# Optimization experiments

Hardware: AMD Instinct MI355X
Metric: run time of the kernel (lower is better)

## Reference

```python
import jax, jax.numpy as jnp
import numpy as np

# OmniNet(deepqmc) reconstruction: ElectronicSchNet v1 (2 interactions, kernel_dim=8,
# embedding_dim=16, dist_feat_dim=4) + Linear(16,1,bias=False) orbital + sum over electrons.
# SchNet v1: shared w and g per interaction, spin-dependent h (same/anti), nuclear
# messages via learned nuclear embeddings Y. Subnets: w = 2-layer log-DNN 4->6->8 with SSP,
# h = Linear(16,8), g = Linear(8,16). SSP(x) = softplus(x) - log(2).

N_UP, N_DOWN = 16, 16
N_ELEC = N_UP + N_DOWN
N_ATOMS = 8
DIST_FEAT, KERNEL, EMBED = 4, 8, 16
N_INTER = 2
BATCH = 4096


def ssp(x):
    return jax.nn.softplus(x) - jnp.log(2.0).astype(x.dtype)


def setup_inputs() -> dict:
    key = jax.random.key(0)
    ks = jax.random.split(key, 16)
    s = 0.5  # init scale
    return {
        'dists_nuc': jax.random.uniform(ks[0], (BATCH, N_ELEC, N_ATOMS, DIST_FEAT), jnp.float32),
        'dists_elec': jax.random.uniform(ks[1], (BATCH, N_ELEC, N_ELEC, DIST_FEAT), jnp.float32),
        'X': jax.random.normal(ks[2], (1, EMBED), jnp.float32) * s,          # electron embedding (n_up==n_down)
        'Y': jax.random.normal(ks[3], (N_ATOMS, KERNEL), jnp.float32) * s,   # nuclear embeddings
        'w1': jax.random.normal(ks[4], (N_INTER, DIST_FEAT, 6), jnp.float32) * s,
        'wb1': jax.random.normal(ks[5], (N_INTER, 6), jnp.float32) * s,
        'w2': jax.random.normal(ks[6], (N_INTER, 6, KERNEL), jnp.float32) * s,
        'wb2': jax.random.normal(ks[7], (N_INTER, KERNEL), jnp.float32) * s,
        'hs_w': jax.random.normal(ks[8], (N_INTER, EMBED, KERNEL), jnp.float32) * s,
        'hs_b': jax.random.normal(ks[9], (N_INTER, KERNEL), jnp.float32) * s,
        'ha_w': jax.random.normal(ks[10], (N_INTER, EMBED, KERNEL), jnp.float32) * s,
        'ha_b': jax.random.normal(ks[11], (N_INTER, KERNEL), jnp.float32) * s,
        'g_w': jax.random.normal(ks[12], (N_INTER, KERNEL, EMBED), jnp.float32) * s,
        'g_b': jax.random.normal(ks[13], (N_INTER, EMBED), jnp.float32) * s,
        'orb_w': jax.random.normal(ks[14], (EMBED,), jnp.float32) * s,
    }


def reference(dists_nuc, dists_elec, X, Y, w1, wb1, w2, wb2, hs_w, hs_b, ha_w, ha_b, g_w, g_b, orb_w):
    B, n_elec = dists_elec.shape[:2]
    dt = dists_elec.dtype
    spins = jnp.concatenate([jnp.zeros(N_UP, jnp.int32), jnp.ones(N_DOWN, jnp.int32)])
    eye = jnp.eye(n_elec, dtype=bool)
    same = ((spins[:, None] == spins[None, :]) & ~eye).astype(dt)  # (i,j) same-spin, no self
    anti = (spins[:, None] != spins[None, :]).astype(dt)

    # initial embeddings: all electrons share X[0] since n_up == n_down
    x = jnp.broadcast_to(X[0], (B, n_elec, EMBED))

    for n in range(N_INTER):
        def w_net(e):  # (..., 4) -> (..., 8)
            return ssp(e @ w1[n] + wb1[n]) @ w2[n] + wb2[n]
        we = w_net(dists_elec)            # (B, i, j, K)
        wn = w_net(dists_nuc)             # (B, i, M, K)
        hs = x @ hs_w[n] + hs_b[n]        # (B, j, K) same-spin message features
        ha = x @ ha_w[n] + ha_b[n]        # (B, j, K) anti-spin
        z = (jnp.einsum('bijk,ij,bjk->bik', we, same, hs)
             + jnp.einsum('bijk,ij,bjk->bik', we, anti, ha)
             + jnp.einsum('bimk,mk->bik', wn, Y))
        x = x + (z @ g_w[n] + g_b[n])     # residual update

    # orbital projection (Linear(16,1,bias=False)), squeeze, sum over electrons
    return (x @ orb_w).sum(axis=-1)       # (B,)
```

## Files before the change

kernel.cpp:

```cpp
#include <hip/hip_runtime.h>

#define NE 32
#define NA 8
#define DF 4
#define KD 8
#define ED 16
#define BATCH 4096

#define WS_W1S0 0
#define WS_W1S1 24
#define WS_B1S0 48
#define WS_B1S1 54
#define WS_B2H0 60
#define WS_B2H1 68
#define WS_MS0  76
#define WS_MA0  84
#define WS_MS   92
#define WS_MA   156
#define WS_CS   220
#define WS_CA   228
#define WS_GO0  236
#define WS_GO1  244
#define WS_BASE 252

__global__ void omni_setup(const float* __restrict__ X,   const float* __restrict__ w1,
                           const float* __restrict__ wb1, const float* __restrict__ w2,
                           const float* __restrict__ wb2, const float* __restrict__ hs_w,
                           const float* __restrict__ hs_b,const float* __restrict__ ha_w,
                           const float* __restrict__ ha_b,const float* __restrict__ g_w,
                           const float* __restrict__ g_b, const float* __restrict__ orb_w,
                           float* __restrict__ ws)
{
    const int t = threadIdx.x;
    const float L   = 1.4426950408889634f;
    const float LN2 = 0.6931471805599453f;
    if (t < 48) {
        ws[t] = w1[t] * L;
    } else if (t < 60) {
        ws[t] = wb1[t - 48] * L;
    } else if (t < 76) {
        const int u = t - 60, n = u >> 3, k = u & 7;
        float sw = 0.f;
        for (int a = 0; a < 6; ++a) sw += w2[n * 48 + a * KD + k];
        ws[t] = wb2[n * KD + k] * L - sw;
    } else if (t < 92) {
        const int u = t - 76, tab = u >> 3, k = u & 7;
        const float* mw = tab ? ha_w : hs_w;
        const float* mb = tab ? ha_b : hs_b;
        float acc = mb[k];
        for (int c = 0; c < ED; ++c) acc += X[c] * mw[c * KD + k];
        ws[t] = acc;
    } else if (t < 220) {
        int u = t - 92; const int tab = u >> 6; u &= 63;
        const int kp = u >> 3, k = u & 7;
        const float* mw = (tab ? ha_w : hs_w) + ED * KD;
        float acc = 0.f;
        for (int c = 0; c < ED; ++c)
            acc += LN2 * g_w[kp * ED + c] * mw[c * KD + k];
        ws[t] = acc;
    } else if (t < 236) {
        const int u = t - 220, tab = u >> 3, k = u & 7;
        const float* mw = (tab ? ha_w : hs_w) + ED * KD;
        const float* mb = (tab ? ha_b : hs_b) + KD;
        float acc = mb[k];
        for (int c = 0; c < ED; ++c) acc += (X[c] + g_b[c]) * mw[c * KD + k];
        ws[t] = acc;
    } else if (t < 252) {
        const int u = t - 236, n = u >> 3, k = u & 7;
        float acc = 0.f;
        for (int c = 0; c < ED; ++c)
            acc += LN2 * g_w[n * KD * ED + k * ED + c] * orb_w[c];
        ws[t] = acc;
    } else if (t == 252) {
        float acc = 0.f;
        for (int c = 0; c < ED; ++c) acc += (X[c] + g_b[c] + g_b[ED + c]) * orb_w[c];
        ws[t] = acc;
    }
}

__device__ __forceinline__ void wnet(const float4 e,
                                     const float* __restrict__ vB1s,
                                     const float* __restrict__ vB2h,
                                     const float* __restrict__ sW1,
                                     const float* __restrict__ sW2,
                                     float* __restrict__ racc)
{
    float r[6];
    #pragma unroll
    for (int a = 0; a < 6; ++a) {
        float u = fmaf(e.x, sW1[a], vB1s[a]);
        u = fmaf(e.y, sW1[6 + a], u);
        u = fmaf(e.z, sW1[12 + a], u);
        u = fmaf(e.w, sW1[18 + a], u);
        r[a] = __builtin_amdgcn_logf(__builtin_amdgcn_exp2f(u) + 1.0f);
    }
    #pragma unroll
    for (int k = 0; k < KD; ++k) {
        float acc = fmaf(r[0], sW2[k], vB2h[k]);
        #pragma unroll
        for (int a = 1; a < 6; ++a) acc = fmaf(r[a], sW2[a * KD + k], acc);
        racc[k] = acc;
    }
}

__global__ __launch_bounds__(128, 4) void omni_main(
    const float* __restrict__ dists_nuc,
    const float* __restrict__ dists_elec,
    const float* __restrict__ Y,
    const float* __restrict__ w2,
    const float* __restrict__ ws,
    float* __restrict__ out)
{
    const int tid  = threadIdx.x;
    const int h    = tid >> 6;
    const int lane = tid & 63;
    const int il   = lane & 15;
    const int jh   = lane >> 4;
    const int ig   = 16 * h + il;
    const int b    = blockIdx.x;
    const int sj   = jh >> 1;
    const bool same = (sj == h);
    const int t32  = same ? 0 : 32;

    __shared__ float msg[65][KD];
    __shared__ float part[2];
    if (tid < KD) msg[64][tid] = 0.0f;

    const float* de = dists_elec + (((size_t)b * NE + ig) * NE + 8 * jh) * DF;
    const float* dn = dists_nuc  + (((size_t)b * NE + ig) * NA + 2 * jh) * DF;
    float4 E[8];
    #pragma unroll
    for (int s = 0; s < 8; ++s) E[s] = ((const float4*)de)[s];
    const float4 F0 = ((const float4*)dn)[0];
    const float4 F1 = ((const float4*)dn)[1];
    const float4 Ya0 = ((const float4*)Y)[4 * jh + 0];
    const float4 Ya1 = ((const float4*)Y)[4 * jh + 1];
    const float4 Yb0 = ((const float4*)Y)[4 * jh + 2];
    const float4 Yb1 = ((const float4*)Y)[4 * jh + 3];

    float zr0[KD];
    {
        float vB1s[6], vB2h[KD], msel[KD];
        #pragma unroll
        for (int a = 0; a < 6; ++a) vB1s[a] = ws[WS_B1S0 + a];
        #pragma unroll
        for (int k = 0; k < KD; ++k) vB2h[k] = ws[WS_B2H0 + k];
        #pragma unroll
        for (int k = 0; k < KD; ++k) msel[k] = same ? ws[WS_MS0 + k] : ws[WS_MA0 + k];

        float zacc[KD];
        #pragma unroll
        for (int k = 0; k < KD; ++k) zacc[k] = 0.0f;
        const int scnt = ig - 8 * jh;
        #pragma unroll
        for (int s = 0; s < 8; ++s) {
            float racc[KD];
            wnet(E[s], vB1s, vB2h, ws + WS_W1S0, w2, racc);
            const float mf = (s == scnt) ? 0.0f : 1.0f;
            #pragma unroll
            for (int k = 0; k < KD; ++k) zacc[k] = fmaf(racc[k], mf, zacc[k]);
        }
        float z[KD];
        #pragma unroll
        for (int k = 0; k < KD; ++k) z[k] = zacc[k] * msel[k];
        {
            float racc[KD];
            wnet(F0, vB1s, vB2h, ws + WS_W1S0, w2, racc);
            z[0] = fmaf(racc[0], Ya0.x, z[0]); z[1] = fmaf(racc[1], Ya0.y, z[1]);
            z[2] = fmaf(racc[2], Ya0.z, z[2]); z[3] = fmaf(racc[3], Ya0.w, z[3]);
            z[4] = fmaf(racc[4], Ya1.x, z[4]); z[5] = fmaf(racc[5], Ya1.y, z[5]);
            z[6] = fmaf(racc[6], Ya1.z, z[6]); z[7] = fmaf(racc[7], Ya1.w, z[7]);
            wnet(F1, vB1s, vB2h, ws + WS_W1S0, w2, racc);
            z[0] = fmaf(racc[0], Yb0.x, z[0]); z[1] = fmaf(racc[1], Yb0.y, z[1]);
            z[2] = fmaf(racc[2], Yb0.z, z[2]); z[3] = fmaf(racc[3], Yb0.w, z[3]);
            z[4] = fmaf(racc[4], Yb1.x, z[4]); z[5] = fmaf(racc[5], Yb1.y, z[5]);
            z[6] = fmaf(racc[6], Yb1.z, z[6]); z[7] = fmaf(racc[7], Yb1.w, z[7]);
        }
        #pragma unroll
        for (int k = 0; k < KD; ++k) {
            z[k] += __shfl_xor(z[k], 16, 64);
            z[k] += __shfl_xor(z[k], 32, 64);
            zr0[k] = z[k];
        }
    }

    {
        float ms[KD], ma[KD];
        #pragma unroll
        for (int k = 0; k < KD; ++k) {
            float as = zr0[0] * ws[WS_MS + k];
            float aa = zr0[0] * ws[WS_MA + k];
            #pragma unroll
            for (int kp = 1; kp < KD; ++kp) {
                as = fmaf(zr0[kp], ws[WS_MS + kp * KD + k], as);
                aa = fmaf(zr0[kp], ws[WS_MA + kp * KD + k], aa);
            }
            ms[k] = as + ws[WS_CS + k];
            ma[k] = aa + ws[WS_CA + k];
        }
        if (jh == 0) {
            #pragma unroll
            for (int k = 0; k < KD; ++k) msg[ig][k] = ms[k];
        } else if (jh == 2) {
            #pragma unroll
            for (int k = 0; k < KD; ++k) msg[32 + ig][k] = ma[k];
        }
        __syncthreads();
    }

    float zr1[KD];
    {
        float vB1s[6], vB2h[KD];
        #pragma unroll
        for (int a = 0; a < 6; ++a) vB1s[a] = ws[WS_B1S1 + a];
        #pragma unroll
        for (int k = 0; k < KD; ++k) vB2h[k] = ws[WS_B2H1 + k];

        float z[KD];
        #pragma unroll
        for (int k = 0; k < KD; ++k) z[k] = 0.0f;
        #pragma unroll
        for (int s = 0; s < 8; ++s) {
            float racc[KD];
            wnet(E[s], vB1s, vB2h, ws + WS_W1S1, w2 + 48, racc);
            const int j = 8 * jh + s;
            const int row = (j == ig) ? 64 : (t32 + j);
            const float4 m0 = *(const float4*)&msg[row][0];
            const float4 m1 = *(const float4*)&msg[row][4];
            z[0] = fmaf(racc[0], m0.x, z[0]); z[1] = fmaf(racc[1], m0.y, z[1]);
            z[2] = fmaf(racc[2], m0.z, z[2]); z[3] = fmaf(racc[3], m0.w, z[3]);
            z[4] = fmaf(racc[4], m1.x, z[4]); z[5] = fmaf(racc[5], m1.y, z[5]);
            z[6] = fmaf(racc[6], m1.z, z[6]); z[7] = fmaf(racc[7], m1.w, z[7]);
        }
        {
            float racc[KD];
            wnet(F0, vB1s, vB2h, ws + WS_W1S1, w2 + 48, racc);
            z[0] = fmaf(racc[0], Ya0.x, z[0]); z[1] = fmaf(racc[1], Ya0.y, z[1]);
            z[2] = fmaf(racc[2], Ya0.z, z[2]); z[3] = fmaf(racc[3], Ya0.w, z[3]);
            z[4] = fmaf(racc[4], Ya1.x, z[4]); z[5] = fmaf(racc[5], Ya1.y, z[5]);
            z[6] = fmaf(racc[6], Ya1.z, z[6]); z[7] = fmaf(racc[7], Ya1.w, z[7]);
            wnet(F1, vB1s, vB2h, ws + WS_W1S1, w2 + 48, racc);
            z[0] = fmaf(racc[0], Yb0.x, z[0]); z[1] = fmaf(racc[1], Yb0.y, z[1]);
            z[2] = fmaf(racc[2], Yb0.z, z[2]); z[3] = fmaf(racc[3], Yb0.w, z[3]);
            z[4] = fmaf(racc[4], Yb1.x, z[4]); z[5] = fmaf(racc[5], Yb1.y, z[5]);
            z[6] = fmaf(racc[6], Yb1.z, z[6]); z[7] = fmaf(racc[7], Yb1.w, z[7]);
        }
        #pragma unroll
        for (int k = 0; k < KD; ++k) {
            z[k] += __shfl_xor(z[k], 16, 64);
            z[k] += __shfl_xor(z[k], 32, 64);
            zr1[k] = z[k];
        }
    }

    float dot = 0.0f;
    #pragma unroll
    for (int k = 0; k < KD; ++k) dot = fmaf(zr0[k], ws[WS_GO0 + k], dot);
    #pragma unroll
    for (int k = 0; k < KD; ++k) dot = fmaf(zr1[k], ws[WS_GO1 + k], dot);
    dot += ws[WS_BASE];
    dot *= 0.25f;
    #pragma unroll
    for (int off = 1; off < 64; off <<= 1) dot += __shfl_xor(dot, off, 64);
    if (lane == 0) part[h] = dot;
    __syncthreads();
    if (tid == 0) out[b] = part[0] + part[1];
}

extern "C" void kernel_launch(void* const* d_in, const int* in_sizes, int n_in,
                              void* d_out, int out_size, void* d_ws, size_t ws_size,
                              hipStream_t stream) {
    const float* dists_nuc  = (const float*)d_in[0];
    const float* dists_elec = (const float*)d_in[1];
    const float* X     = (const float*)d_in[2];
    const float* Y     = (const float*)d_in[3];
    const float* w1    = (const float*)d_in[4];
    const float* wb1   = (const float*)d_in[5];
    const float* w2    = (const float*)d_in[6];
    const float* wb2   = (const float*)d_in[7];
    const float* hs_w  = (const float*)d_in[8];
    const float* hs_b  = (const float*)d_in[9];
    const float* ha_w  = (const float*)d_in[10];
    const float* ha_b  = (const float*)d_in[11];
    const float* g_w   = (const float*)d_in[12];
    const float* g_b   = (const float*)d_in[13];
    const float* orb_w = (const float*)d_in[14];
    float* out = (float*)d_out;
    float* ws  = (float*)d_ws;

    omni_setup<<<1, 256, 0, stream>>>(X, w1, wb1, w2, wb2, hs_w, hs_b,
                                      ha_w, ha_b, g_w, g_b, orb_w, ws);
    omni_main<<<BATCH, 128, 0, stream>>>(dists_nuc, dists_elec, Y, w2, ws, out);
}
```

Baseline: 156.3 us.

## Sum first-interaction SSP features before projection and pack two samples per block

In the first interaction the per-pair message is linear in the SSP hidden layer, so the kernel now sums the six hidden activations over j and applies the 6->8 projection once, scaling the bias by the neighbour count. This removes most of the per-pair projection FMAs. Each 256-thread block now handles two batch samples with separate shared buffers, and launch bounds change to 256 threads with 6 waves. The Y loads are moved into the scopes where they are used to shorten register live ranges. The bias scaling relies on the count being 7 or 8, and the occupancy change may shift register pressure.

```diff
diff --git a/kernel.cpp b/kernel.cpp
--- a/kernel.cpp
+++ b/kernel.cpp
@@ -78,14 +78,11 @@
     }
 }
 
-__device__ __forceinline__ void wnet(const float4 e,
-                                     const float* __restrict__ vB1s,
-                                     const float* __restrict__ vB2h,
-                                     const float* __restrict__ sW1,
-                                     const float* __restrict__ sW2,
-                                     float* __restrict__ racc)
+__device__ __forceinline__ void wnet_r(const float4 e,
+                                       const float* __restrict__ vB1s,
+                                       const float* __restrict__ sW1,
+                                       float* __restrict__ r)
 {
-    float r[6];
     #pragma unroll
     for (int a = 0; a < 6; ++a) {
         float u = fmaf(e.x, sW1[a], vB1s[a]);
@@ -94,6 +91,13 @@
         u = fmaf(e.w, sW1[18 + a], u);
         r[a] = __builtin_amdgcn_logf(__builtin_amdgcn_exp2f(u) + 1.0f);
     }
+}
+
+__device__ __forceinline__ void proj(const float* __restrict__ r,
+                                     const float* __restrict__ sW2,
+                                     const float* __restrict__ vB2h,
+                                     float* __restrict__ racc)
+{
     #pragma unroll
     for (int k = 0; k < KD; ++k) {
         float acc = fmaf(r[0], sW2[k], vB2h[k]);
@@ -103,7 +107,7 @@
     }
 }
 
-__global__ __launch_bounds__(128, 4) void omni_main(
+__global__ __launch_bounds__(256, 6) void omni_main(
     const float* __restrict__ dists_nuc,
     const float* __restrict__ dists_elec,
     const float* __restrict__ Y,
@@ -112,19 +116,20 @@
     float* __restrict__ out)
 {
     const int tid  = threadIdx.x;
-    const int h    = tid >> 6;
+    const int el   = tid >> 7;
+    const int h    = (tid >> 6) & 1;
     const int lane = tid & 63;
     const int il   = lane & 15;
     const int jh   = lane >> 4;
     const int ig   = 16 * h + il;
-    const int b    = blockIdx.x;
+    const int b    = blockIdx.x * 2 + el;
     const int sj   = jh >> 1;
     const bool same = (sj == h);
     const int t32  = same ? 0 : 32;
 
-    __shared__ float msg[65][KD];
-    __shared__ float part[2];
-    if (tid < KD) msg[64][tid] = 0.0f;
+    __shared__ float msg[2][65][KD];
+    __shared__ float part[2][2];
+    if (tid < 16) msg[tid >> 3][64][tid & 7] = 0.0f;
 
     const float* de = dists_elec + (((size_t)b * NE + ig) * NE + 8 * jh) * DF;
     const float* dn = dists_nuc  + (((size_t)b * NE + ig) * NA + 2 * jh) * DF;
@@ -133,10 +138,6 @@
     for (int s = 0; s < 8; ++s) E[s] = ((const float4*)de)[s];
     const float4 F0 = ((const float4*)dn)[0];
     const float4 F1 = ((const float4*)dn)[1];
-    const float4 Ya0 = ((const float4*)Y)[4 * jh + 0];
-    const float4 Ya1 = ((const float4*)Y)[4 * jh + 1];
-    const float4 Yb0 = ((const float4*)Y)[4 * jh + 2];
-    const float4 Yb1 = ((const float4*)Y)[4 * jh + 3];
 
     float zr0[KD];
     {
@@ -148,29 +149,39 @@
         #pragma unroll
         for (int k = 0; k < KD; ++k) msel[k] = same ? ws[WS_MS0 + k] : ws[WS_MA0 + k];
 
-        float zacc[KD];
-        #pragma unroll
-        for (int k = 0; k < KD; ++k) zacc[k] = 0.0f;
         const int scnt = ig - 8 * jh;
+        const float fcnt = (jh == (ig >> 3)) ? 7.0f : 8.0f;
+        float S[6] = {0.f, 0.f, 0.f, 0.f, 0.f, 0.f};
         #pragma unroll
         for (int s = 0; s < 8; ++s) {
-            float racc[KD];
-            wnet(E[s], vB1s, vB2h, ws + WS_W1S0, w2, racc);
+            float r[6];
+            wnet_r(E[s], vB1s, ws + WS_W1S0, r);
             const float mf = (s == scnt) ? 0.0f : 1.0f;
             #pragma unroll
-            for (int k = 0; k < KD; ++k) zacc[k] = fmaf(racc[k], mf, zacc[k]);
+            for (int a = 0; a < 6; ++a) S[a] = fmaf(r[a], mf, S[a]);
         }
         float z[KD];
         #pragma unroll
-        for (int k = 0; k < KD; ++k) z[k] = zacc[k] * msel[k];
+        for (int k = 0; k < KD; ++k) {
+            float acc = fmaf(S[0], w2[k], fcnt * vB2h[k]);
+            #pragma unroll
+            for (int a = 1; a < 6; ++a) acc = fmaf(S[a], w2[a * KD + k], acc);
+            z[k] = acc * msel[k];
+        }
         {
-            float racc[KD];
-            wnet(F0, vB1s, vB2h, ws + WS_W1S0, w2, racc);
+            const float4 Ya0 = ((const float4*)Y)[4 * jh + 0];
+            const float4 Ya1 = ((const float4*)Y)[4 * jh + 1];
+            const float4 Yb0 = ((const float4*)Y)[4 * jh + 2];
+            const float4 Yb1 = ((const float4*)Y)[4 * jh + 3];
+            float r[6], racc[KD];
+            wnet_r(F0, vB1s, ws + WS_W1S0, r);
+            proj(r, w2, vB2h, racc);
             z[0] = fmaf(racc[0], Ya0.x, z[0]); z[1] = fmaf(racc[1], Ya0.y, z[1]);
             z[2] = fmaf(racc[2], Ya0.z, z[2]); z[3] = fmaf(racc[3], Ya0.w, z[3]);
             z[4] = fmaf(racc[4], Ya1.x, z[4]); z[5] = fmaf(racc[5], Ya1.y, z[5]);
             z[6] = fmaf(racc[6], Ya1.z, z[6]); z[7] = fmaf(racc[7], Ya1.w, z[7]);
-            wnet(F1, vB1s, vB2h, ws + WS_W1S0, w2, racc);
+            wnet_r(F1, vB1s, ws + WS_W1S0, r);
+            proj(r, w2, vB2h, racc);
             z[0] = fmaf(racc[0], Yb0.x, z[0]); z[1] = fmaf(racc[1], Yb0.y, z[1]);
             z[2] = fmaf(racc[2], Yb0.z, z[2]); z[3] = fmaf(racc[3], Yb0.w, z[3]);
             z[4] = fmaf(racc[4], Yb1.x, z[4]); z[5] = fmaf(racc[5], Yb1.y, z[5]);
@@ -200,10 +211,10 @@
         }
         if (jh == 0) {
             #pragma unroll
-            for (int k = 0; k < KD; ++k) msg[ig][k] = ms[k];
+            for (int k = 0; k < KD; ++k) msg[el][ig][k] = ms[k];
         } else if (jh == 2) {
             #pragma unroll
-            for (int k = 0; k < KD; ++k) msg[32 + ig][k] = ma[k];
+            for (int k = 0; k < KD; ++k) msg[el][32 + ig][k] = ma[k];
         }
         __syncthreads();
     }
@@ -221,25 +232,32 @@
         for (int k = 0; k < KD; ++k) z[k] = 0.0f;
         #pragma unroll
         for (int s = 0; s < 8; ++s) {
-            float racc[KD];
-            wnet(E[s], vB1s, vB2h, ws + WS_W1S1, w2 + 48, racc);
+            float r[6], racc[KD];
+            wnet_r(E[s], vB1s, ws + WS_W1S1, r);
+            proj(r, w2 + 48, vB2h, racc);
             const int j = 8 * jh + s;
             const int row = (j == ig) ? 64 : (t32 + j);
-            const float4 m0 = *(const float4*)&msg[row][0];
-            const float4 m1 = *(const float4*)&msg[row][4];
+            const float4 m0 = *(const float4*)&msg[el][row][0];
+            const float4 m1 = *(const float4*)&msg[el][row][4];
             z[0] = fmaf(racc[0], m0.x, z[0]); z[1] = fmaf(racc[1], m0.y, z[1]);
             z[2] = fmaf(racc[2], m0.z, z[2]); z[3] = fmaf(racc[3], m0.w, z[3]);
             z[4] = fmaf(racc[4], m1.x, z[4]); z[5] = fmaf(racc[5], m1.y, z[5]);
             z[6] = fmaf(racc[6], m1.z, z[6]); z[7] = fmaf(racc[7], m1.w, z[7]);
         }
         {
-            float racc[KD];
-            wnet(F0, vB1s, vB2h, ws + WS_W1S1, w2 + 48, racc);
+            const float4 Ya0 = ((const float4*)Y)[4 * jh + 0];
+            const float4 Ya1 = ((const float4*)Y)[4 * jh + 1];
+            const float4 Yb0 = ((const float4*)Y)[4 * jh + 2];
+            const float4 Yb1 = ((const float4*)Y)[4 * jh + 3];
+            float r[6], racc[KD];
+            wnet_r(F0, vB1s, ws + WS_W1S1, r);
+            proj(r, w2 + 48, vB2h, racc);
             z[0] = fmaf(racc[0], Ya0.x, z[0]); z[1] = fmaf(racc[1], Ya0.y, z[1]);
             z[2] = fmaf(racc[2], Ya0.z, z[2]); z[3] = fmaf(racc[3], Ya0.w, z[3]);
             z[4] = fmaf(racc[4], Ya1.x, z[4]); z[5] = fmaf(racc[5], Ya1.y, z[5]);
             z[6] = fmaf(racc[6], Ya1.z, z[6]); z[7] = fmaf(racc[7], Ya1.w, z[7]);
-            wnet(F1, vB1s, vB2h, ws + WS_W1S1, w2 + 48, racc);
+            wnet_r(F1, vB1s, ws + WS_W1S1, r);
+            proj(r, w2 + 48, vB2h, racc);
             z[0] = fmaf(racc[0], Yb0.x, z[0]); z[1] = fmaf(racc[1], Yb0.y, z[1]);
             z[2] = fmaf(racc[2], Yb0.z, z[2]); z[3] = fmaf(racc[3], Yb0.w, z[3]);
             z[4] = fmaf(racc[4], Yb1.x, z[4]); z[5] = fmaf(racc[5], Yb1.y, z[5]);
@@ -262,9 +280,9 @@
     dot *= 0.25f;
     #pragma unroll
     for (int off = 1; off < 64; off <<= 1) dot += __shfl_xor(dot, off, 64);
-    if (lane == 0) part[h] = dot;
+    if (lane == 0) part[el][h] = dot;
     __syncthreads();
-    if (tid == 0) out[b] = part[0] + part[1];
+    if ((tid & 127) == 0) out[b] = part[el][0] + part[el][1];
 }
 
 extern "C" void kernel_launch(void* const* d_in, const int* in_sizes, int n_in,
@@ -290,5 +308,5 @@
 
     omni_setup<<<1, 256, 0, stream>>>(X, w1, wb1, w2, wb2, hs_w, hs_b,
                                       ha_w, ha_b, g_w, g_b, orb_w, ws);
-    omni_main<<<BATCH, 128, 0, stream>>>(dists_nuc, dists_elec, Y, w2, ws, out);
-}
+    omni_main<<<BATCH / 2, 256, 0, stream>>>(dists_nuc, dists_elec, Y, w2, ws, out);
+}
```

Measured after the change: 163.6 us. +4.6%, slower.

## Pack FMAs into float2 ops and hoist interaction-0 projection out of loop

Applied to the files above, without the earlier changes.

Rewrites the w-net and the message projections with 2-wide float vectors so the compiler can emit packed FP32 FMA instructions, which halves the FMA instruction count. In interaction 0 the second linear layer is applied once to the masked sum of hidden activations, scaled by the neighbor count for the bias, instead of once per electron pair. This removes most of that layer's per-pair work. The risks are packed-math codegen overhead from operand splats and register pressure, plus small changes in floating-point summation order.

```diff
diff --git a/kernel.cpp b/kernel.cpp
--- a/kernel.cpp
+++ b/kernel.cpp
@@ -22,6 +22,12 @@
 #define WS_GO0  236
 #define WS_GO1  244
 #define WS_BASE 252
+
+typedef float f32x2 __attribute__((ext_vector_type(2)));
+__device__ __forceinline__ f32x2 splat2(float s) { f32x2 r; r.x = s; r.y = s; return r; }
+__device__ __forceinline__ f32x2 fma2(f32x2 a, f32x2 b, f32x2 c) {
+    return __builtin_elementwise_fma(a, b, c);
+}
 
 __global__ void omni_setup(const float* __restrict__ X,   const float* __restrict__ w1,
                            const float* __restrict__ wb1, const float* __restrict__ w2,
@@ -78,28 +84,41 @@
     }
 }
 
-__device__ __forceinline__ void wnet(const float4 e,
-                                     const float* __restrict__ vB1s,
-                                     const float* __restrict__ vB2h,
-                                     const float* __restrict__ sW1,
-                                     const float* __restrict__ sW2,
-                                     float* __restrict__ racc)
+__device__ __forceinline__ void wnet_r2(const float4 e,
+                                        const f32x2* __restrict__ vB1s2,
+                                        const f32x2* __restrict__ sW12,
+                                        f32x2* __restrict__ r2)
 {
-    float r[6];
-    #pragma unroll
-    for (int a = 0; a < 6; ++a) {
-        float u = fmaf(e.x, sW1[a], vB1s[a]);
-        u = fmaf(e.y, sW1[6 + a], u);
-        u = fmaf(e.z, sW1[12 + a], u);
-        u = fmaf(e.w, sW1[18 + a], u);
-        r[a] = __builtin_amdgcn_logf(__builtin_amdgcn_exp2f(u) + 1.0f);
-    }
-    #pragma unroll
-    for (int k = 0; k < KD; ++k) {
-        float acc = fmaf(r[0], sW2[k], vB2h[k]);
-        #pragma unroll
-        for (int a = 1; a < 6; ++a) acc = fmaf(r[a], sW2[a * KD + k], acc);
-        racc[k] = acc;
+    #pragma unroll
+    for (int a2 = 0; a2 < 3; ++a2) {
+        f32x2 u = fma2(splat2(e.x), sW12[a2], vB1s2[a2]);
+        u = fma2(splat2(e.y), sW12[3 + a2], u);
+        u = fma2(splat2(e.z), sW12[6 + a2], u);
+        u = fma2(splat2(e.w), sW12[9 + a2], u);
+        f32x2 t;
+        t.x = __builtin_amdgcn_exp2f(u.x);
+        t.y = __builtin_amdgcn_exp2f(u.y);
+        t = t + splat2(1.0f);
+        r2[a2].x = __builtin_amdgcn_logf(t.x);
+        r2[a2].y = __builtin_amdgcn_logf(t.y);
+    }
+}
+
+__device__ __forceinline__ void proj2(const f32x2* __restrict__ r2,
+                                      const f32x2* __restrict__ sW22,
+                                      const f32x2* __restrict__ vB2h2,
+                                      f32x2* __restrict__ racc2)
+{
+    #pragma unroll
+    for (int k2 = 0; k2 < 4; ++k2) {
+        f32x2 acc = vB2h2[k2];
+        acc = fma2(splat2(r2[0].x), sW22[0 * 4 + k2], acc);
+        acc = fma2(splat2(r2[0].y), sW22[1 * 4 + k2], acc);
+        acc = fma2(splat2(r2[1].x), sW22[2 * 4 + k2], acc);
+        acc = fma2(splat2(r2[1].y), sW22[3 * 4 + k2], acc);
+        acc = fma2(splat2(r2[2].x), sW22[4 * 4 + k2], acc);
+        acc = fma2(splat2(r2[2].y), sW22[5 * 4 + k2], acc);
+        racc2[k2] = acc;
     }
 }
 
@@ -126,6 +145,10 @@
     __shared__ float part[2];
     if (tid < KD) msg[64][tid] = 0.0f;
 
+    const f32x2* ws2  = (const f32x2*)ws;
+    const f32x2* w2p0 = (const f32x2*)w2;
+    const f32x2* w2p1 = (const f32x2*)(w2 + 48);
+
     const float* de = dists_elec + (((size_t)b * NE + ig) * NE + 8 * jh) * DF;
     const float* dn = dists_nuc  + (((size_t)b * NE + ig) * NA + 2 * jh) * DF;
     float4 E[8];
@@ -133,123 +156,130 @@
     for (int s = 0; s < 8; ++s) E[s] = ((const float4*)de)[s];
     const float4 F0 = ((const float4*)dn)[0];
     const float4 F1 = ((const float4*)dn)[1];
-    const float4 Ya0 = ((const float4*)Y)[4 * jh + 0];
-    const float4 Ya1 = ((const float4*)Y)[4 * jh + 1];
-    const float4 Yb0 = ((const float4*)Y)[4 * jh + 2];
-    const float4 Yb1 = ((const float4*)Y)[4 * jh + 3];
+    f32x2 Y0[4], Y1[4];
+    #pragma unroll
+    for (int k2 = 0; k2 < 4; ++k2) {
+        Y0[k2] = ((const f32x2*)Y)[(2 * jh) * 4 + k2];
+        Y1[k2] = ((const f32x2*)Y)[(2 * jh + 1) * 4 + k2];
+    }
 
     float zr0[KD];
     {
-        float vB1s[6], vB2h[KD], msel[KD];
-        #pragma unroll
-        for (int a = 0; a < 6; ++a) vB1s[a] = ws[WS_B1S0 + a];
-        #pragma unroll
-        for (int k = 0; k < KD; ++k) vB2h[k] = ws[WS_B2H0 + k];
-        #pragma unroll
-        for (int k = 0; k < KD; ++k) msel[k] = same ? ws[WS_MS0 + k] : ws[WS_MA0 + k];
-
-        float zacc[KD];
-        #pragma unroll
-        for (int k = 0; k < KD; ++k) zacc[k] = 0.0f;
-        const int scnt = ig - 8 * jh;
+        f32x2 vB1s2[3], vB2h2[4], msel2[4];
+        #pragma unroll
+        for (int a2 = 0; a2 < 3; ++a2) vB1s2[a2] = ws2[WS_B1S0 / 2 + a2];
+        #pragma unroll
+        for (int k2 = 0; k2 < 4; ++k2) vB2h2[k2] = ws2[WS_B2H0 / 2 + k2];
+        #pragma unroll
+        for (int k2 = 0; k2 < 4; ++k2)
+            msel2[k2] = same ? ws2[WS_MS0 / 2 + k2] : ws2[WS_MA0 / 2 + k2];
+
+        const int scnt  = ig - 8 * jh;
+        const float fcnt = (jh == (ig >> 3)) ? 7.0f : 8.0f;
+        f32x2 S2[3] = {splat2(0.f), splat2(0.f), splat2(0.f)};
         #pragma unroll
         for (int s = 0; s < 8; ++s) {
-            float racc[KD];
-            wnet(E[s], vB1s, vB2h, ws + WS_W1S0, w2, racc);
+            f32x2 r2[3];
+            wnet_r2(E[s], vB1s2, ws2 + WS_W1S0 / 2, r2);
             const float mf = (s == scnt) ? 0.0f : 1.0f;
             #pragma unroll
-            for (int k = 0; k < KD; ++k) zacc[k] = fmaf(racc[k], mf, zacc[k]);
-        }
-        float z[KD];
-        #pragma unroll
-        for (int k = 0; k < KD; ++k) z[k] = zacc[k] * msel[k];
+            for (int a2 = 0; a2 < 3; ++a2) S2[a2] = fma2(r2[a2], splat2(mf), S2[a2]);
+        }
+        f32x2 z2[4];
+        #pragma unroll
+        for (int k2 = 0; k2 < 4; ++k2) {
+            f32x2 acc = splat2(fcnt) * vB2h2[k2];
+            acc = fma2(splat2(S2[0].x), w2p0[0 * 4 + k2], acc);
+            acc = fma2(splat2(S2[0].y), w2p0[1 * 4 + k2], acc);
+            acc = fma2(splat2(S2[1].x), w2p0[2 * 4 + k2], acc);
+            acc = fma2(splat2(S2[1].y), w2p0[3 * 4 + k2], acc);
+            acc = fma2(splat2(S2[2].x), w2p0[4 * 4 + k2], acc);
+            acc = fma2(splat2(S2[2].y), w2p0[5 * 4 + k2], acc);
+            z2[k2] = acc * msel2[k2];
+        }
         {
-            float racc[KD];
-            wnet(F0, vB1s, vB2h, ws + WS_W1S0, w2, racc);
-            z[0] = fmaf(racc[0], Ya0.x, z[0]); z[1] = fmaf(racc[1], Ya0.y, z[1]);
-            z[2] = fmaf(racc[2], Ya0.z, z[2]); z[3] = fmaf(racc[3], Ya0.w, z[3]);
-            z[4] = fmaf(racc[4], Ya1.x, z[4]); z[5] = fmaf(racc[5], Ya1.y, z[5]);
-            z[6] = fmaf(racc[6], Ya1.z, z[6]); z[7] = fmaf(racc[7], Ya1.w, z[7]);
-            wnet(F1, vB1s, vB2h, ws + WS_W1S0, w2, racc);
-            z[0] = fmaf(racc[0], Yb0.x, z[0]); z[1] = fmaf(racc[1], Yb0.y, z[1]);
-            z[2] = fmaf(racc[2], Yb0.z, z[2]); z[3] = fmaf(racc[3], Yb0.w, z[3]);
-            z[4] = fmaf(racc[4], Yb1.x, z[4]); z[5] = fmaf(racc[5], Yb1.y, z[5]);
-            z[6] = fmaf(racc[6], Yb1.z, z[6]); z[7] = fmaf(racc[7], Yb1.w, z[7]);
-        }
-        #pragma unroll
-        for (int k = 0; k < KD; ++k) {
-            z[k] += __shfl_xor(z[k], 16, 64);
-            z[k] += __shfl_xor(z[k], 32, 64);
-            zr0[k] = z[k];
+            f32x2 r2[3], racc2[4];
+            wnet_r2(F0, vB1s2, ws2 + WS_W1S0 / 2, r2);
+            proj2(r2, w2p0, vB2h2, racc2);
+            #pragma unroll
+            for (int k2 = 0; k2 < 4; ++k2) z2[k2] = fma2(racc2[k2], Y0[k2], z2[k2]);
+            wnet_r2(F1, vB1s2, ws2 + WS_W1S0 / 2, r2);
+            proj2(r2, w2p0, vB2h2, racc2);
+            #pragma unroll
+            for (int k2 = 0; k2 < 4; ++k2) z2[k2] = fma2(racc2[k2], Y1[k2], z2[k2]);
+        }
+        #pragma unroll
+        for (int k2 = 0; k2 < 4; ++k2) {
+            float za = z2[k2].x, zb = z2[k2].y;
+            za += __shfl_xor(za, 16, 64); za += __shfl_xor(za, 32, 64);
+            zb += __shfl_xor(zb, 16, 64); zb += __shfl_xor(zb, 32, 64);
+            zr0[2 * k2] = za; zr0[2 * k2 + 1] = zb;
         }
     }
 
     {
-        float ms[KD], ma[KD];
-        #pragma unroll
-        for (int k = 0; k < KD; ++k) {
-            float as = zr0[0] * ws[WS_MS + k];
-            float aa = zr0[0] * ws[WS_MA + k];
-            #pragma unroll
-            for (int kp = 1; kp < KD; ++kp) {
-                as = fmaf(zr0[kp], ws[WS_MS + kp * KD + k], as);
-                aa = fmaf(zr0[kp], ws[WS_MA + kp * KD + k], aa);
+        f32x2 ms2[4], ma2[4];
+        #pragma unroll
+        for (int k2 = 0; k2 < 4; ++k2) {
+            ms2[k2] = ws2[WS_CS / 2 + k2];
+            ma2[k2] = ws2[WS_CA / 2 + k2];
+        }
+        #pragma unroll
+        for (int kp = 0; kp < KD; ++kp) {
+            const f32x2 zk = splat2(zr0[kp]);
+            #pragma unroll
+            for (int k2 = 0; k2 < 4; ++k2) {
+                ms2[k2] = fma2(zk, ws2[WS_MS / 2 + kp * 4 + k2], ms2[k2]);
+                ma2[k2] = fma2(zk, ws2[WS_MA / 2 + kp * 4 + k2], ma2[k2]);
             }
-            ms[k] = as + ws[WS_CS + k];
-            ma[k] = aa + ws[WS_CA + k];
         }
         if (jh == 0) {
             #pragma unroll
-            for (int k = 0; k < KD; ++k) msg[ig][k] = ms[k];
+            for (int k2 = 0; k2 < 4; ++k2) *(f32x2*)&msg[ig][2 * k2] = ms2[k2];
         } else if (jh == 2) {
             #pragma unroll
-            for (int k = 0; k < KD; ++k) msg[32 + ig][k] = ma[k];
+            for (int k2 = 0; k2 < 4; ++k2) *(f32x2*)&msg[32 + ig][2 * k2] = ma2[k2];
         }
         __syncthreads();
     }
 
     float zr1[KD];
     {
-        float vB1s[6], vB2h[KD];
-        #pragma unroll
-        for (int a = 0; a < 6; ++a) vB1s[a] = ws[WS_B1S1 + a];
-        #pragma unroll
-        for (int k = 0; k < KD; ++k) vB2h[k] = ws[WS_B2H1 + k];
-
-        float z[KD];
-        #pragma unroll
-        for (int k = 0; k < KD; ++k) z[k] = 0.0f;
+        f32x2 vB1s2[3], vB2h2[4];
+        #pragma unroll
+        for (int a2 = 0; a2 < 3; ++a2) vB1s2[a2] = ws2[WS_B1S1 / 2 + a2];
+        #pragma unroll
+        for (int k2 = 0; k2 < 4; ++k2) vB2h2[k2] = ws2[WS_B2H1 / 2 + k2];
+
+        f32x2 z2[4] = {splat2(0.f), splat2(0.f), splat2(0.f), splat2(0.f)};
         #pragma unroll
         for (int s = 0; s < 8; ++s) {
-            float racc[KD];
-            wnet(E[s], vB1s, vB2h, ws + WS_W1S1, w2 + 48, racc);
+            f32x2 r2[3], racc2[4];
+            wnet_r2(E[s], vB1s2, ws2 + WS_W1S1 / 2, r2);
+            proj2(r2, w2p1, vB2h2, racc2);
             const int j = 8 * jh + s;
             const int row = (j == ig) ? 64 : (t32 + j);
-            const float4 m0 = *(const float4*)&msg[row][0];
-            const float4 m1 = *(const float4*)&msg[row][4];
-            z[0] = fmaf(racc[0], m0.x, z[0]); z[1] = fmaf(racc[1], m0.y, z[1]);
-            z[2] = fmaf(racc[2], m0.z, z[2]); z[3] = fmaf(racc[3], m0.w, z[3]);
-            z[4] = fmaf(racc[4], m1.x, z[4]); z[5] = fmaf(racc[5], m1.y, z[5]);
-            z[6] = fmaf(racc[6], m1.z, z[6]); z[7] = fmaf(racc[7], m1.w, z[7]);
+            const f32x2* mrow = (const f32x2*)&msg[row][0];
+            #pragma unroll
+            for (int k2 = 0; k2 < 4; ++k2) z2[k2] = fma2(racc2[k2], mrow[k2], z2[k2]);
         }
         {
-            float racc[KD];
-            wnet(F0, vB1s, vB2h, ws + WS_W1S1, w2 + 48, racc);
-            z[0] = fmaf(racc[0], Ya0.x, z[0]); z[1] = fmaf(racc[1], Ya0.y, z[1]);
-            z[2] = fmaf(racc[2], Ya0.z, z[2]); z[3] = fmaf(racc[3], Ya0.w, z[3]);
-            z[4] = fmaf(racc[4], Ya1.x, z[4]); z[5] = fmaf(racc[5], Ya1.y, z[5]);
-            z[6] = fmaf(racc[6], Ya1.z, z[6]); z[7] = fmaf(racc[7], Ya1.w, z[7]);
-            wnet(F1, vB1s, vB2h, ws + WS_W1S1, w2 + 48, racc);
-            z[0] = fmaf(racc[0], Yb0.x, z[0]); z[1] = fmaf(racc[1], Yb0.y, z[1]);
-            z[2] = fmaf(racc[2], Yb0.z, z[2]); z[3] = fmaf(racc[3], Yb0.w, z[3]);
-            z[4] = fmaf(racc[4], Yb1.x, z[4]); z[5] = fmaf(racc[5], Yb1.y, z[5]);
-            z[6] = fmaf(racc[6], Yb1.z, z[6]); z[7] = fmaf(racc[7], Yb1.w, z[7]);
-        }
-        #pragma unroll
-        for (int k = 0; k < KD; ++k) {
-            z[k] += __shfl_xor(z[k], 16, 64);
-            z[k] += __shfl_xor(z[k], 32, 64);
-            zr1[k] = z[k];
+            f32x2 r2[3], racc2[4];
+            wnet_r2(F0, vB1s2, ws2 + WS_W1S1 / 2, r2);
+            proj2(r2, w2p1, vB2h2, racc2);
+            #pragma unroll
+            for (int k2 = 0; k2 < 4; ++k2) z2[k2] = fma2(racc2[k2], Y0[k2], z2[k2]);
+            wnet_r2(F1, vB1s2, ws2 + WS_W1S1 / 2, r2);
+            proj2(r2, w2p1, vB2h2, racc2);
+            #pragma unroll
+            for (int k2 = 0; k2 < 4; ++k2) z2[k2] = fma2(racc2[k2], Y1[k2], z2[k2]);
+        }
+        #pragma unroll
+        for (int k2 = 0; k2 < 4; ++k2) {
+            float za = z2[k2].x, zb = z2[k2].y;
+            za += __shfl_xor(za, 16, 64); za += __shfl_xor(za, 32, 64);
+            zb += __shfl_xor(zb, 16, 64); zb += __shfl_xor(zb, 32, 64);
+            zr1[2 * k2] = za; zr1[2 * k2 + 1] = zb;
         }
     }
 
```

New measurement: 157.4 us. About the same (+0.7%).
